# Performance work log

Hardware: AMD Instinct MI355X
Metric: run time of the kernel (lower is better)

## Reference

```python
import jax, jax.numpy as jnp
import numpy as np

B, T, E, H, D = 4, 2048, 1024, 16, 64  # batch, seq (==context), embed, heads, head_size


def setup_inputs() -> dict:
    key = jax.random.key(0)
    ks = jax.random.split(key, 5)
    s_in = 1.0 / np.sqrt(E)
    s_c = 1.0 / np.sqrt(H * D)
    return {
        "x": jax.random.normal(ks[0], (B, T, E), dtype=jnp.float32),
        "Wq": jax.random.normal(ks[1], (H, E, D), dtype=jnp.float32) * s_in,
        "Wk": jax.random.normal(ks[2], (H, E, D), dtype=jnp.float32) * s_in,
        "Wv": jax.random.normal(ks[3], (H, E, D), dtype=jnp.float32) * s_in,
        "Wc": jax.random.normal(ks[4], (H * D, E), dtype=jnp.float32) * s_c,
    }


def reference(x, Wq, Wk, Wv, Wc):
    # Batched equivalent of the per-head Python loop: each head h does
    # q = x @ Wq[h], k = x @ Wk[h], v = x @ Wv[h]; causal softmax attention.
    q = jnp.einsum("bse,hed->bhsd", x, Wq)
    k = jnp.einsum("bte,hed->bhtd", x, Wk)
    v = jnp.einsum("bte,hed->bhtd", x, Wv)
    scale = 1.0 / jnp.sqrt(jnp.asarray(D, dtype=x.dtype))
    scores = jnp.einsum("bhsd,bhtd->bhst", q, k) * scale  # [B,H,T,T]
    causal = jnp.tril(jnp.ones((T, T), dtype=bool))
    scores = jnp.where(causal[None, None], scores, jnp.asarray(-jnp.inf, dtype=scores.dtype))
    attn = jax.nn.softmax(scores, axis=-1)
    out = jnp.einsum("bhst,bhtd->bhsd", attn, v)
    # concat heads along last dim (head 0 first), then combine linear
    out = out.transpose(0, 2, 1, 3).reshape(B, T, H * D)
    return out @ Wc
```

## Files before the change

kernel.cpp:

```cpp
#include <hip/hip_runtime.h>
#include <cstdint>
#include <cstddef>

typedef unsigned short u16;
typedef __bf16 bf16x8 __attribute__((ext_vector_type(8)));
typedef float f32x4 __attribute__((ext_vector_type(4)));
typedef float f32x16 __attribute__((ext_vector_type(16)));

#define B_ 4
#define T_ 2048
#define E_ 1024
#define H_ 16
#define D_ 64
#define HD3_ 3072
#define M_ (B_*T_)

__device__ __forceinline__ u16 f2bf(float f) {
  union { float f; unsigned u; } v; v.f = f;
  unsigned r = v.u + 0x7FFFu + ((v.u >> 16) & 1u);
  return (u16)(r >> 16);
}

__device__ __forceinline__ unsigned cvtpk(float a, float b) {
  unsigned r;
  asm("v_cvt_pk_bf16_f32 %0, %1, %2" : "=v"(r) : "v"(a), "v"(b));
  return r;
}

__device__ __forceinline__ void gl2lds16(const u16* g, u16* l) {
  __builtin_amdgcn_global_load_lds(
      (const __attribute__((address_space(1))) unsigned int*)g,
      (__attribute__((address_space(3))) unsigned int*)l, 16, 0, 0);
}

__global__ void prep_x(const float* __restrict__ x, u16* __restrict__ xb) {
  const long n4 = (long)(M_) * E_ / 4;
  for (long i = (long)blockIdx.x * blockDim.x + threadIdx.x; i < n4;
       i += (long)gridDim.x * blockDim.x) {
    float4 v = ((const float4*)x)[i];
    unsigned lo = (unsigned)f2bf(v.x) | ((unsigned)f2bf(v.y) << 16);
    unsigned hi = (unsigned)f2bf(v.z) | ((unsigned)f2bf(v.w) << 16);
    ((uint2*)xb)[i] = make_uint2(lo, hi);
  }
}

__global__ void prep_w(const float* __restrict__ Wq, const float* __restrict__ Wk,
                       const float* __restrict__ Wv, const float* __restrict__ Wc,
                       u16* __restrict__ WT, u16* __restrict__ WcT) {
  const int total = HD3_ * E_ + E_ * E_;
  for (int i = blockIdx.x * blockDim.x + threadIdx.x; i < total;
       i += gridDim.x * blockDim.x) {
    if (i < HD3_ * E_) {
      int n = i >> 10, e = i & 1023;
      int mtx = n >> 10, hd = n & 1023, h = hd >> 6, d = hd & 63;
      const float* W = (mtx == 0) ? Wq : (mtx == 1) ? Wk : Wv;
      WT[i] = f2bf(W[((size_t)h * E_ + e) * D_ + d]);
    } else {
      int j = i - HD3_ * E_;
      int n = j >> 10, k = j & 1023;
      WcT[j] = f2bf(Wc[(size_t)k * E_ + n]);
    }
  }
}

template<bool OUT_BF16>
__global__ __launch_bounds__(256) void gemm_bt(
    const u16* __restrict__ A, const u16* __restrict__ Bt,
    void* __restrict__ Cv, int K, int ldc, int qcols, float qscale)
{
  __shared__ u16 As[128 * 32];
  __shared__ u16 Bs[128 * 32];
  const int tid = threadIdx.x;
  const int lane = tid & 63, w = tid >> 6;
  const int wr = (w >> 1) * 64, wc = (w & 1) * 64;
  const int lrow = lane & 15, lk8 = (lane >> 4) * 8;
  int lin = blockIdx.y * gridDim.x + blockIdx.x;
  int cpx = (gridDim.x * gridDim.y) >> 3;
  int swz = (lin & 7) * cpx + (lin >> 3);
  int bxi = swz % gridDim.x, byi = swz / gridDim.x;
  const long bm = (long)byi * 128;
  const long bn = (long)bxi * 128;
  f32x4 acc[4][4] = {};

  for (int k0 = 0; k0 < K; k0 += 32) {
    __syncthreads();
#pragma unroll
    for (int i = 0; i < 2; ++i) {
      int c = i * 256 + tid, r = c >> 2, cc = c & 3;
      gl2lds16(A + (size_t)(bm + r) * K + k0 + cc * 8, &As[c * 8]);
    }
#pragma unroll
    for (int i = 0; i < 2; ++i) {
      int c = i * 256 + tid, r = c >> 2, cc = c & 3;
      gl2lds16(Bt + (size_t)(bn + r) * K + k0 + cc * 8, &Bs[c * 8]);
    }
    __syncthreads();
    bf16x8 af[4], bfr[4];
#pragma unroll
    for (int mi = 0; mi < 4; ++mi)
      af[mi] = *(const bf16x8*)&As[(wr + mi * 16 + lrow) * 32 + lk8];
#pragma unroll
    for (int ni = 0; ni < 4; ++ni)
      bfr[ni] = *(const bf16x8*)&Bs[(wc + ni * 16 + lrow) * 32 + lk8];
#pragma unroll
    for (int mi = 0; mi < 4; ++mi)
#pragma unroll
      for (int ni = 0; ni < 4; ++ni)
        acc[mi][ni] = __builtin_amdgcn_mfma_f32_16x16x32_bf16(
            af[mi], bfr[ni], acc[mi][ni], 0, 0, 0);
  }

#pragma unroll
  for (int mi = 0; mi < 4; ++mi)
#pragma unroll
    for (int ni = 0; ni < 4; ++ni) {
      long row = bm + wr + mi * 16 + (lane >> 4) * 4;
      long col = bn + wc + ni * 16 + lrow;
      float sc = (col < qcols) ? qscale : 1.0f;
#pragma unroll
      for (int j = 0; j < 4; ++j) {
        if (OUT_BF16)
          ((u16*)Cv)[(size_t)(row + j) * ldc + col] = f2bf(acc[mi][ni][j] * sc);
        else
          ((float*)Cv)[(size_t)(row + j) * ldc + col] = acc[mi][ni][j];
      }
    }
}

__global__ __launch_bounds__(256) void transpose_v(const u16* __restrict__ QKV,
                                                   u16* __restrict__ VT) {
  const int bh = blockIdx.y, b = bh >> 4, h = bh & 15;
  const int t0 = blockIdx.x * 64;
  __shared__ u16 tile[64][72];
  const int tid = threadIdx.x;
  const u16* src = QKV + ((size_t)(b * T_ + t0) * HD3_ + 2048 + h * 64);
#pragma unroll
  for (int i = 0; i < 2; ++i) {
    int c = i * 256 + tid;
    int r = c >> 3, cc = (c & 7) * 8;
    uint4 v = *(const uint4*)(src + (size_t)r * HD3_ + cc);
    *(uint4*)&tile[r][cc] = v;
  }
  __syncthreads();
  u16* dst = VT + (size_t)bh * D_ * T_ + t0;
#pragma unroll
  for (int i = 0; i < 16; ++i) {
    int idx = i * 256 + tid;
    int d = idx >> 6, tl = idx & 63;
    dst[(size_t)d * T_ + tl] = tile[tl][d];
  }
}

__global__ __launch_bounds__(256, 2) void attn_kernel(
    const u16* __restrict__ QKV, const u16* __restrict__ VT,
    u16* __restrict__ O)
{
  __shared__ u16 Ks[2][4096];
  __shared__ u16 Vs[2][4096];
  const int L = blockIdx.x;
  const int bh = L & 63, b = bh >> 4, h = bh & 15;
  const int qt = 15 - (L >> 6);
  const int q0 = qt * 128;
  const int tid = threadIdx.x, w = tid >> 6, lane = tid & 63;
  const int ql = lane & 31, hi = lane >> 5;
  const int qw0 = q0 + w * 32;

  const u16* Qg = QKV + ((size_t)(b * T_ + q0) * HD3_ + h * 64);
  const u16* Kg = QKV + ((size_t)(b * T_) * HD3_ + 1024 + h * 64);
  const u16* Vg = VT + (size_t)bh * (D_ * T_);

#pragma unroll
  for (int i = 0; i < 4; ++i) {
    int c = i * 256 + tid, r = c >> 3, cc = c & 7, sc = cc ^ (r & 7);
    gl2lds16(Qg + (size_t)r * HD3_ + sc * 8, &Ks[0][0] + c * 8);
  }
  __syncthreads();
  bf16x8 qf[4];
  {
    int qrow = w * 32 + ql;
#pragma unroll
    for (int s = 0; s < 4; ++s) {
      int ch = (2 * s + hi) ^ (qrow & 7);
      qf[s] = *(const bf16x8*)(&Ks[0][0] + qrow * 64 + ch * 8);
    }
  }
  __syncthreads();

#pragma unroll
  for (int i = 0; i < 2; ++i) {
    int c = i * 256 + tid, r = c >> 3, cc = c & 7, sc = cc ^ (r & 7);
    gl2lds16(Kg + (size_t)r * HD3_ + sc * 8, &Ks[0][0] + c * 8);
    gl2lds16(Vg + (size_t)r * T_ + sc * 8, &Vs[0][0] + c * 8);
  }

  f32x16 acc[2];
#pragma unroll
  for (int ni = 0; ni < 2; ++ni)
#pragma unroll
    for (int r = 0; r < 16; ++r) acc[ni][r] = 0.f;
  float mrun = -1e30f, lrun = 0.f;
  const int ktmax = 2 * qt + 2;

  for (int kt = 0; kt < ktmax; ++kt) {
    const int cur = kt & 1;
    const int kv0 = kt * 64;
    __syncthreads();
    if (kt + 1 < ktmax) {
      const int nkv = kv0 + 64;
#pragma unroll
      for (int i = 0; i < 2; ++i) {
        int c = i * 256 + tid, r = c >> 3, cc = c & 7, sc = cc ^ (r & 7);
        gl2lds16(Kg + (size_t)(nkv + r) * HD3_ + sc * 8, &Ks[cur ^ 1][0] + c * 8);
        gl2lds16(Vg + (size_t)r * T_ + nkv + sc * 8, &Vs[cur ^ 1][0] + c * 8);
      }
    }
    if (kv0 > qw0 + 31) continue;

    f32x16 st[2];
#pragma unroll
    for (int f = 0; f < 2; ++f)
#pragma unroll
      for (int r = 0; r < 16; ++r) st[f][r] = 0.f;
    __builtin_amdgcn_s_setprio(1);
#pragma unroll
    for (int f = 0; f < 2; ++f) {
      const int krow = f * 32 + ql;
      const int swzr = krow & 7;
#pragma unroll
      for (int s = 0; s < 4; ++s) {
        int ch = (2 * s + hi) ^ swzr;
        bf16x8 kfr = *(const bf16x8*)(&Ks[cur][0] + krow * 64 + ch * 8);
        st[f] = __builtin_amdgcn_mfma_f32_32x32x16_bf16(kfr, qf[s], st[f], 0, 0, 0);
      }
    }
    __builtin_amdgcn_s_setprio(0);

    if (kv0 + 63 > qw0) {
      const int qg = qw0 + ql;
#pragma unroll
      for (int f = 0; f < 2; ++f)
#pragma unroll
        for (int r = 0; r < 16; ++r) {
          int kg = kv0 + f * 32 + (r & 3) + 8 * (r >> 2) + 4 * hi;
          if (kg > qg) st[f][r] = -1e30f;
        }
    }

    float mt = st[0][0];
#pragma unroll
    for (int f = 0; f < 2; ++f)
#pragma unroll
      for (int r = 0; r < 16; ++r) mt = fmaxf(mt, st[f][r]);
    mt = fmaxf(mt, __shfl_xor(mt, 32, 64));
    if (!__all(mt - mrun <= 8.f)) {
      float mnew = fmaxf(mrun, mt);
      float corr = exp2f(mrun - mnew);
      lrun *= corr;
#pragma unroll
      for (int ni = 0; ni < 2; ++ni)
#pragma unroll
        for (int r = 0; r < 16; ++r) acc[ni][r] *= corr;
      mrun = mnew;
    }
    float sum = 0.f;
#pragma unroll
    for (int f = 0; f < 2; ++f)
#pragma unroll
      for (int r = 0; r < 16; ++r) {
        float p = exp2f(st[f][r] - mrun);
        st[f][r] = p;
        sum += p;
      }
    sum += __shfl_xor(sum, 32, 64);
    lrun += sum;

    __builtin_amdgcn_s_setprio(1);
#pragma unroll
    for (int s = 0; s < 4; ++s) {
      const int f = s >> 1, bse = (s & 1) * 8;
      unsigned b0 = cvtpk(st[f][bse + 0], st[f][bse + 1]);
      unsigned b1 = cvtpk(st[f][bse + 2], st[f][bse + 3]);
      unsigned a0 = cvtpk(st[f][bse + 4], st[f][bse + 5]);
      unsigned a1 = cvtpk(st[f][bse + 6], st[f][bse + 7]);
      asm volatile("v_permlane32_swap_b32 %0, %1" : "+v"(b0), "+v"(a0));
      asm volatile("v_permlane32_swap_b32 %0, %1" : "+v"(b1), "+v"(a1));
      union { unsigned u[4]; bf16x8 v; } pa;
      pa.u[0] = b0; pa.u[1] = b1; pa.u[2] = a0; pa.u[3] = a1;
#pragma unroll
      for (int ni = 0; ni < 2; ++ni) {
        int vrow = ni * 32 + ql;
        int ch = (2 * s + hi) ^ (vrow & 7);
        bf16x8 vf = *(const bf16x8*)(&Vs[cur][0] + vrow * 64 + ch * 8);
        acc[ni] = __builtin_amdgcn_mfma_f32_32x32x16_bf16(vf, pa.v, acc[ni], 0, 0, 0);
      }
    }
    __builtin_amdgcn_s_setprio(0);
  }

  const int q = q0 + w * 32 + ql;
  u16* Og = O + ((size_t)(b * T_ + q) * (H_ * D_) + h * 64);
  const float inv = 1.f / lrun;
#pragma unroll
  for (int ni = 0; ni < 2; ++ni)
#pragma unroll
    for (int rr = 0; rr < 8; ++rr) {
      const int r0 = rr * 2;
      const int d0 = ((r0 & 3) + 8 * (r0 >> 2)) + 4 * hi + ni * 32;
      unsigned pk = cvtpk(acc[ni][r0] * inv, acc[ni][r0 + 1] * inv);
      *(unsigned*)(Og + d0) = pk;
    }
}

extern "C" void kernel_launch(void* const* d_in, const int* in_sizes, int n_in,
                              void* d_out, int out_size, void* d_ws, size_t ws_size,
                              hipStream_t stream) {
  const float* x  = (const float*)d_in[0];
  const float* Wq = (const float*)d_in[1];
  const float* Wk = (const float*)d_in[2];
  const float* Wv = (const float*)d_in[3];
  const float* Wc = (const float*)d_in[4];

  char* ws = (char*)d_ws;
  u16* xb  = (u16*)(ws);
  u16* WT  = (u16*)(ws + 16777216);
  u16* WcT = (u16*)(ws + 23068672);
  u16* QKV = (u16*)(ws + 25165824);
  u16* Ob  = (u16*)(ws + 75497472);
  u16* VT  = xb;
  float* out = (float*)d_out;

  const float QSCALE = 0.125f * 1.4426950408889634f;

  prep_x<<<2048, 256, 0, stream>>>(x, xb);
  prep_w<<<4096, 256, 0, stream>>>(Wq, Wk, Wv, Wc, WT, WcT);
  gemm_bt<true><<<dim3(24, 64), 256, 0, stream>>>(xb, WT, QKV, 1024, 3072, 1024, QSCALE);
  transpose_v<<<dim3(32, 64), 256, 0, stream>>>(QKV, VT);
  attn_kernel<<<dim3(1024), 256, 0, stream>>>(QKV, VT, Ob);
  gemm_bt<false><<<dim3(8, 64), 256, 0, stream>>>(Ob, WcT, out, 1024, 1024, 0, 1.0f);
}
```

Measured before the change: 280.2 us.

## Rewrite projection GEMMs with double-buffered swizzled LDS and 128x256 tiles

Replaces the single-buffered 128x128, K=32 GEMM with a 512-thread, 128x256-tile kernel. It uses K=64 steps, double-buffered LDS with XOR-swizzled layout to avoid bank conflicts, and interleaved global-to-LDS prefetch split across two MFMA phases. Barriers, waitcnt and setprio are placed by hand. The goal is to hide global load latency and raise MFMA utilisation for the QKV and output projections. In exchange, the kernel is hardcoded to K=1024 and the manual vmcnt accounting is fragile. The larger LDS footprint of about 96KB may also limit occupancy.

```diff
diff --git a/kernel.cpp b/kernel.cpp
--- a/kernel.cpp
+++ b/kernel.cpp
@@ -63,66 +63,134 @@
   }
 }
 
-template<bool OUT_BF16>
-__global__ __launch_bounds__(256) void gemm_bt(
+template<int N_, bool OUT_BF16>
+__global__ __launch_bounds__(512, 2) void gemm8(
     const u16* __restrict__ A, const u16* __restrict__ Bt,
-    void* __restrict__ Cv, int K, int ldc, int qcols, float qscale)
+    void* __restrict__ Cv, float qscale)
 {
-  __shared__ u16 As[128 * 32];
-  __shared__ u16 Bs[128 * 32];
+  __shared__ u16 As[2][128 * 64];
+  __shared__ u16 Bs[2][256 * 64];
   const int tid = threadIdx.x;
   const int lane = tid & 63, w = tid >> 6;
-  const int wr = (w >> 1) * 64, wc = (w & 1) * 64;
-  const int lrow = lane & 15, lk8 = (lane >> 4) * 8;
-  int lin = blockIdx.y * gridDim.x + blockIdx.x;
-  int cpx = (gridDim.x * gridDim.y) >> 3;
-  int swz = (lin & 7) * cpx + (lin >> 3);
-  int bxi = swz % gridDim.x, byi = swz / gridDim.x;
-  const long bm = (long)byi * 128;
-  const long bn = (long)bxi * 128;
+  const int wr = w >> 2, wc = w & 3;
+  const int l15 = lane & 15, l4 = lane >> 4;
+
+  const int gx = N_ / 256;
+  const int lin = blockIdx.x;
+  const int cpx = (gx * 64) >> 3;
+  const int swz = (lin & 7) * cpx + (lin >> 3);
+  const int bxi = swz % gx, byi = swz / gx;
+  const size_t bm = (size_t)byi * 128, bn = (size_t)bxi * 256;
+  const u16* Ag = A + bm * 1024;
+  const u16* Bg = Bt + bn * 1024;
+
+  auto stageA = [&](int b, int t, int i) {
+    int idx = i * 512 + tid, r = idx >> 3, c = idx & 7;
+    gl2lds16(Ag + (size_t)r * 1024 + t * 64 + ((c ^ (r & 7)) * 8), &As[b][idx * 8]);
+  };
+  auto stageB = [&](int b, int t, int i) {
+    int idx = i * 512 + tid, r = idx >> 3, c = idx & 7;
+    gl2lds16(Bg + (size_t)r * 1024 + t * 64 + ((c ^ (r & 7)) * 8), &Bs[b][idx * 8]);
+  };
+
+  int aoff[4][2], boff[4][2];
+#pragma unroll
+  for (int m = 0; m < 4; ++m) {
+    int r = wr * 64 + m * 16 + l15;
+#pragma unroll
+    for (int s = 0; s < 2; ++s)
+      aoff[m][s] = r * 64 + (((s * 4 + l4) ^ (r & 7)) * 8);
+  }
+#pragma unroll
+  for (int n = 0; n < 4; ++n) {
+    int r = wc * 64 + n * 16 + l15;
+#pragma unroll
+    for (int s = 0; s < 2; ++s)
+      boff[n][s] = r * 64 + (((s * 4 + l4) ^ (r & 7)) * 8);
+  }
+
   f32x4 acc[4][4] = {};
 
-  for (int k0 = 0; k0 < K; k0 += 32) {
-    __syncthreads();
-#pragma unroll
-    for (int i = 0; i < 2; ++i) {
-      int c = i * 256 + tid, r = c >> 2, cc = c & 3;
-      gl2lds16(A + (size_t)(bm + r) * K + k0 + cc * 8, &As[c * 8]);
-    }
-#pragma unroll
-    for (int i = 0; i < 2; ++i) {
-      int c = i * 256 + tid, r = c >> 2, cc = c & 3;
-      gl2lds16(Bt + (size_t)(bn + r) * K + k0 + cc * 8, &Bs[c * 8]);
-    }
-    __syncthreads();
-    bf16x8 af[4], bfr[4];
-#pragma unroll
-    for (int mi = 0; mi < 4; ++mi)
-      af[mi] = *(const bf16x8*)&As[(wr + mi * 16 + lrow) * 32 + lk8];
-#pragma unroll
-    for (int ni = 0; ni < 4; ++ni)
-      bfr[ni] = *(const bf16x8*)&Bs[(wc + ni * 16 + lrow) * 32 + lk8];
-#pragma unroll
-    for (int mi = 0; mi < 4; ++mi)
-#pragma unroll
-      for (int ni = 0; ni < 4; ++ni)
-        acc[mi][ni] = __builtin_amdgcn_mfma_f32_16x16x32_bf16(
-            af[mi], bfr[ni], acc[mi][ni], 0, 0, 0);
-  }
-
-#pragma unroll
-  for (int mi = 0; mi < 4; ++mi)
-#pragma unroll
-    for (int ni = 0; ni < 4; ++ni) {
-      long row = bm + wr + mi * 16 + (lane >> 4) * 4;
-      long col = bn + wc + ni * 16 + lrow;
-      float sc = (col < qcols) ? qscale : 1.0f;
+#pragma unroll
+  for (int i = 0; i < 2; ++i) stageA(0, 0, i);
+#pragma unroll
+  for (int i = 0; i < 4; ++i) stageB(0, 0, i);
+#pragma unroll
+  for (int i = 0; i < 2; ++i) stageA(1, 1, i);
+  asm volatile("s_waitcnt vmcnt(2)" ::: "memory");
+  __builtin_amdgcn_s_barrier();
+
+  for (int t = 0; t < 16; ++t) {
+    const int cur = t & 1;
+    bf16x8 af[4][2], bfv[4][2];
+#pragma unroll
+    for (int m = 0; m < 4; ++m)
+#pragma unroll
+      for (int s = 0; s < 2; ++s)
+        af[m][s] = *(const bf16x8*)&As[cur][aoff[m][s]];
+#pragma unroll
+    for (int n = 0; n < 2; ++n)
+#pragma unroll
+      for (int s = 0; s < 2; ++s)
+        bfv[n][s] = *(const bf16x8*)&Bs[cur][boff[n][s]];
+    if (t + 1 < 16) {
+      stageB(cur ^ 1, t + 1, 0);
+      stageB(cur ^ 1, t + 1, 1);
+      stageB(cur ^ 1, t + 1, 2);
+    }
+    __builtin_amdgcn_s_barrier();
+    asm volatile("s_waitcnt lgkmcnt(0)" ::: "memory");
+    __builtin_amdgcn_sched_barrier(0);
+    __builtin_amdgcn_s_setprio(1);
+#pragma unroll
+    for (int m = 0; m < 4; ++m)
+#pragma unroll
+      for (int n = 0; n < 2; ++n)
+#pragma unroll
+        for (int s = 0; s < 2; ++s)
+          acc[m][n] = __builtin_amdgcn_mfma_f32_16x16x32_bf16(
+              af[m][s], bfv[n][s], acc[m][n], 0, 0, 0);
+    __builtin_amdgcn_s_setprio(0);
+    __builtin_amdgcn_s_barrier();
+
+#pragma unroll
+    for (int n = 2; n < 4; ++n)
+#pragma unroll
+      for (int s = 0; s < 2; ++s)
+        bfv[n][s] = *(const bf16x8*)&Bs[cur][boff[n][s]];
+    if (t + 1 < 16) stageB(cur ^ 1, t + 1, 3);
+    if (t + 2 < 16) { stageA(cur, t + 2, 0); stageA(cur, t + 2, 1); }
+    __builtin_amdgcn_s_barrier();
+    asm volatile("s_waitcnt lgkmcnt(0)" ::: "memory");
+    __builtin_amdgcn_sched_barrier(0);
+    __builtin_amdgcn_s_setprio(1);
+#pragma unroll
+    for (int m = 0; m < 4; ++m)
+#pragma unroll
+      for (int n = 2; n < 4; ++n)
+#pragma unroll
+        for (int s = 0; s < 2; ++s)
+          acc[m][n] = __builtin_amdgcn_mfma_f32_16x16x32_bf16(
+              af[m][s], bfv[n][s], acc[m][n], 0, 0, 0);
+    __builtin_amdgcn_s_setprio(0);
+    if (t + 2 < 16)      asm volatile("s_waitcnt vmcnt(2)" ::: "memory");
+    else if (t + 1 < 16) asm volatile("s_waitcnt vmcnt(0)" ::: "memory");
+    __builtin_amdgcn_s_barrier();
+  }
+
+#pragma unroll
+  for (int m = 0; m < 4; ++m)
+#pragma unroll
+    for (int n = 0; n < 4; ++n) {
+      size_t row = bm + wr * 64 + m * 16 + l4 * 4;
+      size_t col = bn + wc * 64 + n * 16 + l15;
+      float sc = (col < 1024) ? qscale : 1.0f;
 #pragma unroll
       for (int j = 0; j < 4; ++j) {
         if (OUT_BF16)
-          ((u16*)Cv)[(size_t)(row + j) * ldc + col] = f2bf(acc[mi][ni][j] * sc);
+          ((u16*)Cv)[(row + j) * N_ + col] = f2bf(acc[m][n][j] * sc);
         else
-          ((float*)Cv)[(size_t)(row + j) * ldc + col] = acc[mi][ni][j];
+          ((float*)Cv)[(row + j) * N_ + col] = acc[m][n][j];
       }
     }
 }
@@ -333,8 +401,8 @@
 
   prep_x<<<2048, 256, 0, stream>>>(x, xb);
   prep_w<<<4096, 256, 0, stream>>>(Wq, Wk, Wv, Wc, WT, WcT);
-  gemm_bt<true><<<dim3(24, 64), 256, 0, stream>>>(xb, WT, QKV, 1024, 3072, 1024, QSCALE);
+  gemm8<3072, true><<<768, 512, 0, stream>>>(xb, WT, QKV, QSCALE);
   transpose_v<<<dim3(32, 64), 256, 0, stream>>>(QKV, VT);
   attn_kernel<<<dim3(1024), 256, 0, stream>>>(QKV, VT, Ob);
-  gemm_bt<false><<<dim3(8, 64), 256, 0, stream>>>(Ob, WcT, out, 1024, 1024, 0, 1.0f);
-}
+  gemm8<1024, false><<<256, 512, 0, stream>>>(Ob, WcT, out, 1.0f);
+}
```

Measured after the change: 266.8 us. 1.05x faster.
